# Performance work log

Measured on AMD Instinct MI355X. Metric: run time of the kernel, lower is better.

The kernel has to match this reference:

```python
import jax, jax.numpy as jnp
import numpy as np

B, S, D = 2, 2048, 2048
H, KV, HD = 32, 8, 64          # n_heads, n_kv_heads, head_dim
REP = H // KV                  # 4
THETA = 10000.0


def _rotate_half(u):
    h = u.shape[-1] // 2
    return jnp.concatenate([-u[..., h:], u[..., :h]], axis=-1)


def setup_inputs() -> dict:
    key = jax.random.key(0)
    ks = jax.random.split(key, 5)
    x = jax.random.normal(ks[0], (B, S, D), dtype=jnp.float32)
    Wq = jax.random.normal(ks[1], (D, H * HD), dtype=jnp.float32) * 0.02
    Wk = jax.random.normal(ks[2], (D, KV * HD), dtype=jnp.float32) * 0.02
    Wv = jax.random.normal(ks[3], (D, KV * HD), dtype=jnp.float32) * 0.02
    Wo = jax.random.normal(ks[4], (H * HD, D), dtype=jnp.float32) * 0.02
    return {"x": x, "Wq": Wq, "Wk": Wk, "Wv": Wv, "Wo": Wo}


def reference(x, Wq, Wk, Wv, Wo):
    b, s, d = x.shape
    # QKV projections (nn.Linear, no bias)
    q = (x @ Wq).reshape(b, s, H, HD).transpose(0, 2, 1, 3)   # [B,H,S,HD]
    k = (x @ Wk).reshape(b, s, KV, HD).transpose(0, 2, 1, 3)  # [B,KV,S,HD]
    v = (x @ Wv).reshape(b, s, KV, HD).transpose(0, 2, 1, 3)  # [B,KV,S,HD]

    # RoPE (position_offset = 0)
    inv_freq = 1.0 / (THETA ** (jnp.arange(0, HD, 2, dtype=jnp.float32) / HD))
    freqs = jnp.outer(jnp.arange(s, dtype=jnp.float32), inv_freq)  # [S,HD/2]
    emb = jnp.concatenate([freqs, freqs], axis=-1)                  # [S,HD]
    cos, sin = jnp.cos(emb), jnp.sin(emb)
    q = q * cos + _rotate_half(q) * sin
    k = k * cos + _rotate_half(k) * sin

    # Grouped attention: avoid materializing repeated KV tensors.
    qg = q.reshape(b, KV, REP, s, HD)                               # [B,KV,REP,S,HD]
    scale = 1.0 / np.sqrt(HD)
    scores = jnp.einsum('bgrqd,bgkd->bgrqk', qg, k) * scale         # [B,KV,REP,S,S]
    causal = jnp.tril(jnp.ones((s, s), dtype=bool))
    scores = jnp.where(causal, scores, jnp.finfo(jnp.float32).min)
    probs = jax.nn.softmax(scores.astype(jnp.float32), axis=-1).astype(q.dtype)
    out = jnp.einsum('bgrqk,bgkd->bgrqd', probs, v)                 # [B,KV,REP,S,HD]
    out = out.reshape(b, H, s, HD).transpose(0, 2, 1, 3).reshape(b, s, H * HD)
    return out @ Wo                                                  # [B,S,D]
```

## Files before the change

### kernel.cpp

```cpp
#include <hip/hip_runtime.h>
#include <math.h>

typedef __bf16 bf16_t;
typedef bf16_t bf16x8 __attribute__((ext_vector_type(8)));
typedef bf16_t bf16x4 __attribute__((ext_vector_type(4)));
typedef float floatx4 __attribute__((ext_vector_type(4)));
typedef short short4v __attribute__((ext_vector_type(4)));

#define MFMA16(a, b, c) __builtin_amdgcn_mfma_f32_16x16x32_bf16((a), (b), (c), 0, 0, 0)

#if __has_builtin(__builtin_amdgcn_exp2f)
#define PEXP(x) __builtin_amdgcn_exp2f(x)
#define SCORE_SCALE (0.125f * 1.4426950408889634f)
#else
#define PEXP(x) __expf(x)
#define SCORE_SCALE 0.125f
#endif

#if __has_builtin(__builtin_amdgcn_mfma_f32_16x16x16bf16_1k)
#define HAVE_MFMA_K16 1
__device__ __forceinline__ floatx4 mfma_k16(bf16x4 a, bf16x4 b, floatx4 c)
{
    union { bf16x4 v; short4v s; } ua, ub;
    ua.v = a; ub.v = b;
    return __builtin_amdgcn_mfma_f32_16x16x16bf16_1k(ua.s, ub.s, c, 0, 0, 0);
}
#endif

union PU { unsigned u[2]; bf16x4 v; };
union BU { unsigned u[4]; bf16x8 v; };

__device__ __forceinline__ void gld16(const void* g, void* lds)
{
    __builtin_amdgcn_global_load_lds(
        reinterpret_cast<const __attribute__((address_space(1))) void*>(
            reinterpret_cast<uintptr_t>(g)),
        reinterpret_cast<__attribute__((address_space(3))) void*>(
            (unsigned int)reinterpret_cast<uintptr_t>(lds)),
        16, 0, 0);
}

template <typename TC>
__device__ __forceinline__ void gemm_bt_body(
    const bf16_t* __restrict__ A, const bf16_t* __restrict__ Bt,
    TC* __restrict__ C, int row0, int col0, int N, int K,
    bf16_t* As, bf16_t* Bs)
{
    const int tid  = threadIdx.x;
    const int wave = tid >> 6, lane = tid & 63;
    const int quad = lane >> 4, l16 = lane & 15;
    const int wm = (wave >> 1) * 64, wn = (wave & 1) * 64;

    floatx4 acc[4][4] = {};

    for (int k0 = 0; k0 < K; k0 += 64) {
        __syncthreads();
        #pragma unroll
        for (int i = 0; i < 4; ++i) {
            int c = i * 256 + tid;
            int r = c >> 3, s = c & 7;
            int ks = k0 + ((s ^ (r & 7)) << 3);
            gld16(A  + (size_t)(row0 + r) * K + ks, &As[(i * 256 + wave * 64) * 8]);
            gld16(Bt + (size_t)(col0 + r) * K + ks, &Bs[(i * 256 + wave * 64) * 8]);
        }
        __syncthreads();
        #pragma unroll
        for (int kh = 0; kh < 2; ++kh) {
            bf16x8 af[4], bfr[4];
            #pragma unroll
            for (int t = 0; t < 4; ++t) {
                int ar = wm + t * 16 + l16;
                af[t]  = *(const bf16x8*)&As[ar * 64 + (((kh * 4 + quad) ^ (ar & 7)) << 3)];
                int br = wn + t * 16 + l16;
                bfr[t] = *(const bf16x8*)&Bs[br * 64 + (((kh * 4 + quad) ^ (br & 7)) << 3)];
            }
            #pragma unroll
            for (int mt = 0; mt < 4; ++mt)
                #pragma unroll
                for (int nt = 0; nt < 4; ++nt)
                    acc[mt][nt] = MFMA16(af[mt], bfr[nt], acc[mt][nt]);
        }
    }
    #pragma unroll
    for (int mt = 0; mt < 4; ++mt)
        #pragma unroll
        for (int nt = 0; nt < 4; ++nt)
            #pragma unroll
            for (int r = 0; r < 4; ++r)
                C[(size_t)(row0 + wm + mt * 16 + quad * 4 + r) * N
                  + col0 + wn + nt * 16 + l16] = (TC)acc[mt][nt][r];
}

template <typename TC>
__global__ __launch_bounds__(256) void gemm_bt(
    const bf16_t* __restrict__ A, const bf16_t* __restrict__ Bt,
    TC* __restrict__ C, int N, int K)
{
    __shared__ bf16_t As[128 * 64];
    __shared__ bf16_t Bs[128 * 64];
    gemm_bt_body<TC>(A, Bt, C, blockIdx.y * 128, blockIdx.x * 128, N, K, As, Bs);
}

__global__ __launch_bounds__(256) void gemm_qkv(
    const bf16_t* __restrict__ A, const bf16_t* __restrict__ BtQ,
    const bf16_t* __restrict__ BtK, const bf16_t* __restrict__ BtV,
    bf16_t* __restrict__ CQ, bf16_t* __restrict__ CK, bf16_t* __restrict__ CV)
{
    __shared__ bf16_t As[128 * 64];
    __shared__ bf16_t Bs[128 * 64];
    const int x = blockIdx.x;
    const bf16_t* Bt; bf16_t* C; int N, col0;
    if (x < 16)      { Bt = BtQ; C = CQ; N = 2048; col0 = x * 128; }
    else if (x < 20) { Bt = BtK; C = CK; N = 512;  col0 = (x - 16) * 128; }
    else             { Bt = BtV; C = CV; N = 512;  col0 = (x - 20) * 128; }
    gemm_bt_body<bf16_t>(A, Bt, C, blockIdx.y * 128, col0, N, 2048, As, Bs);
}

__device__ __forceinline__ void transpose_body(
    const float* __restrict__ W, bf16_t* __restrict__ Wt, int K, int N,
    int bx, int by, float (*t)[33], int tid)
{
    int tx = tid & 31, ty = tid >> 5;
    #pragma unroll
    for (int i = 0; i < 32; i += 8)
        t[ty + i][tx] = W[(size_t)(by + ty + i) * N + bx + tx];
    __syncthreads();
    #pragma unroll
    for (int i = 0; i < 32; i += 8)
        Wt[(size_t)(bx + ty + i) * K + by + tx] = (bf16_t)t[tx][ty + i];
}

__global__ __launch_bounds__(256) void prep_all(
    const float* __restrict__ x, const float* __restrict__ Wq,
    const float* __restrict__ Wk, const float* __restrict__ Wv,
    bf16_t* __restrict__ xb, bf16_t* __restrict__ WqT,
    bf16_t* __restrict__ WkT, bf16_t* __restrict__ WvT)
{
    __shared__ float t[32][33];
    const int blk = blockIdx.x, tid = threadIdx.x;
    if (blk < 8192) {
        int i = blk * 256 + tid;
        float4 f = ((const float4*)x)[i];
        bf16x4 v = {(bf16_t)f.x, (bf16_t)f.y, (bf16_t)f.z, (bf16_t)f.w};
        ((bf16x4*)xb)[i] = v;
    } else if (blk < 12288) {
        int r = blk - 8192;
        transpose_body(Wq, WqT, 2048, 2048, (r & 63) * 32, (r >> 6) * 32, t, tid);
    } else if (blk < 13312) {
        int r = blk - 12288;
        transpose_body(Wk, WkT, 2048, 512, (r & 15) * 32, (r >> 4) * 32, t, tid);
    } else {
        int r = blk - 13312;
        transpose_body(Wv, WvT, 2048, 512, (r & 15) * 32, (r >> 4) * 32, t, tid);
    }
}

__global__ __launch_bounds__(256) void mid_all(
    bf16_t* __restrict__ Kw, const bf16_t* __restrict__ Vw,
    bf16_t* __restrict__ VtG, const float* __restrict__ Wo,
    bf16_t* __restrict__ WoT)
{
    __shared__ float tf[32][33];
    __shared__ bf16_t tb[32][34];
    const int blk = blockIdx.x, tid = threadIdx.x;
    if (blk < 4096) {
        int idx = blk * 256 + tid;
        int i   = idx & 31;
        int h   = (idx >> 5) & 7;
        int row = idx >> 8;
        int pos = row & 2047;
        float invf = powf(10000.0f, -(float)i / 32.0f);
        float sv, cv;
        sincosf((float)pos * invf, &sv, &cv);
        size_t base = (size_t)row * 512 + (size_t)h * 64 + i;
        float a  = (float)Kw[base];
        float b2 = (float)Kw[base + 32];
        Kw[base]      = (bf16_t)(a * cv - b2 * sv);
        Kw[base + 32] = (bf16_t)(b2 * cv + a * sv);
    } else if (blk < 6144) {
        int r  = blk - 4096;
        int bz = r >> 10, r2 = r & 1023;
        int bx = (r2 & 15) * 32, by = (r2 >> 4) * 32;
        int tx = tid & 31, ty = tid >> 5;
        #pragma unroll
        for (int i = 0; i < 32; i += 8)
            tb[ty + i][tx] = Vw[((size_t)bz * 2048 + by + ty + i) * 512 + bx + tx];
        __syncthreads();
        #pragma unroll
        for (int i = 0; i < 32; i += 8)
            VtG[((size_t)bz * 512 + bx + ty + i) * 2048 + by + tx] = tb[tx][ty + i];
    } else {
        int r = blk - 6144;
        transpose_body(Wo, WoT, 2048, 2048, (r & 63) * 32, (r >> 6) * 32, tf, tid);
    }
}

__global__ __launch_bounds__(256) void gqa_attn(
    const bf16_t* __restrict__ Q, const bf16_t* __restrict__ Kc,
    const bf16_t* __restrict__ Vt, bf16_t* __restrict__ AO)
{
    __shared__ alignas(16) bf16_t Ks[2][64 * 64];
    __shared__ alignas(16) bf16_t Vs[2][64 * 64];

    const int x = blockIdx.x, h = blockIdx.y, b = blockIdx.z, g = h >> 2;
    const int tid  = threadIdx.x;
    const int wave = tid >> 6, lane = tid & 63;
    const int quad = lane >> 4, l16 = lane & 15;

    #pragma unroll 1
    for (int t = 0; t < 2; ++t) {
        const int qt = t ? x : (15 - x);
        const int q0 = qt * 128;
        int qb[2];
        qb[0] = q0 + wave * 16;
        qb[1] = qb[0] + 64;

        bf16x8 qf[2][2];
        #pragma unroll
        for (int mt = 0; mt < 2; ++mt) {
            int qrow = qb[mt] + l16;
            const bf16_t* qp = Q + (size_t)(b * 2048 + qrow) * 2048 + h * 64 + quad * 8;
            bf16x8 lo = *(const bf16x8*)qp;
            bf16x8 hi = *(const bf16x8*)(qp + 32);
            #pragma unroll
            for (int j = 0; j < 8; ++j) {
                int d = quad * 8 + j;
                float invf = powf(10000.0f, -(float)d / 32.0f);
                float sv, cv;
                sincosf((float)qrow * invf, &sv, &cv);
                float a = (float)lo[j], c2 = (float)hi[j];
                qf[mt][0][j] = (bf16_t)((a * cv - c2 * sv) * SCORE_SCALE);
                qf[mt][1][j] = (bf16_t)((c2 * cv + a * sv) * SCORE_SCALE);
            }
        }

        floatx4 o[2][4] = {};
        floatx4 ls4[2] = {};

        const int ktmax = 2 * qt + 1;

        __asm__ volatile("s_waitcnt lgkmcnt(0)" ::: "memory");
        __builtin_amdgcn_s_barrier();
        #pragma unroll
        for (int i = 0; i < 2; ++i) {
            int c = i * 256 + tid;
            int r = c >> 3, s = c & 7;
            int sw = (s ^ (r & 7)) << 3;
            gld16(Kc + (size_t)(b * 2048 + r) * 512 + g * 64 + sw,
                  &Ks[0][(i * 256 + wave * 64) * 8]);
            gld16(Vt + (size_t)(b * 512 + g * 64 + r) * 2048 + sw,
                  &Vs[0][(i * 256 + wave * 64) * 8]);
        }

        #pragma unroll 1
        for (int kt = 0; kt <= ktmax; ++kt) {
            const int cur = kt & 1;
            if (kt < ktmax) {
                const int kn = kt + 1;
                #pragma unroll
                for (int i = 0; i < 2; ++i) {
                    int c = i * 256 + tid;
                    int r = c >> 3, s = c & 7;
                    int sw = (s ^ (r & 7)) << 3;
                    gld16(Kc + (size_t)(b * 2048 + kn * 64 + r) * 512 + g * 64 + sw,
                          &Ks[cur ^ 1][(i * 256 + wave * 64) * 8]);
                    gld16(Vt + (size_t)(b * 512 + g * 64 + r) * 2048 + kn * 64 + sw,
                          &Vs[cur ^ 1][(i * 256 + wave * 64) * 8]);
                }
                __asm__ volatile("s_waitcnt vmcnt(4)" ::: "memory");
            } else {
                __asm__ volatile("s_waitcnt vmcnt(0)" ::: "memory");
            }
            __builtin_amdgcn_s_barrier();

            bool en[2];
            en[0] = (kt * 64) <= (qb[0] + 15);
            en[1] = (kt * 64) <= (qb[1] + 15);

            floatx4 st[2][4] = {};
            #pragma unroll
            for (int nt = 0; nt < 4; ++nt) {
                int kr = nt * 16 + l16;
                bf16x8 kf0 = *(const bf16x8*)&Ks[cur][kr * 64 + ((quad ^ (kr & 7)) << 3)];
                bf16x8 kf1 = *(const bf16x8*)&Ks[cur][kr * 64 + (((4 + quad) ^ (kr & 7)) << 3)];
                if (en[0]) {
                    st[0][nt] = MFMA16(kf0, qf[0][0], st[0][nt]);
                    st[0][nt] = MFMA16(kf1, qf[0][1], st[0][nt]);
                }
                if (en[1]) {
                    st[1][nt] = MFMA16(kf0, qf[1][0], st[1][nt]);
                    st[1][nt] = MFMA16(kf1, qf[1][1], st[1][nt]);
                }
            }

            PU pk[2][4];
            #pragma unroll
            for (int mt = 0; mt < 2; ++mt) {
                if (!en[mt]) continue;
                const bool diag = (kt * 64 + 63) > qb[mt];
                const int qa = qb[mt] + l16;
                #pragma unroll
                for (int nt = 0; nt < 4; ++nt) {
                    float pv[4];
                    #pragma unroll
                    for (int r = 0; r < 4; ++r) {
                        float e = PEXP(st[mt][nt][r]);
                        if (diag) {
                            int ka = kt * 64 + nt * 16 + quad * 4 + r;
                            if (ka > qa) e = 0.f;
                        }
                        ls4[mt][r] += e;
                        pv[r] = e;
                    }
                    pk[mt][nt].v = bf16x4{(bf16_t)pv[0], (bf16_t)pv[1],
                                          (bf16_t)pv[2], (bf16_t)pv[3]};
                }
            }

#ifdef HAVE_MFMA_K16
            #pragma unroll
            for (int nt = 0; nt < 4; ++nt)
                #pragma unroll
                for (int dt = 0; dt < 4; ++dt) {
                    int vr = dt * 16 + l16;
                    int slot = ((nt << 1) | (quad >> 1)) ^ (vr & 7);
                    bf16x4 va = *(const bf16x4*)&Vs[cur][vr * 64 + (slot << 3)
                                                         + ((quad & 1) << 2)];
                    if (en[0]) o[0][dt] = mfma_k16(va, pk[0][nt].v, o[0][dt]);
                    if (en[1]) o[1][dt] = mfma_k16(va, pk[1][nt].v, o[1][dt]);
                }
#else
            #pragma unroll
            for (int H = 0; H < 2; ++H) {
                BU bfv[2];
                #pragma unroll
                for (int mt = 0; mt < 2; ++mt) {
                    if (!en[mt]) continue;
                    #pragma unroll
                    for (int j = 0; j < 4; ++j) {
                        int srcl = (((quad & 1) << 1) + (j >> 1)) * 16 + l16;
                        unsigned a0 = (unsigned)__shfl((int)pk[mt][2 * H].u[j & 1], srcl, 64);
                        unsigned a1 = (unsigned)__shfl((int)pk[mt][2 * H + 1].u[j & 1], srcl, 64);
                        bfv[mt].u[j] = (quad >> 1) ? a1 : a0;
                    }
                }
                #pragma unroll
                for (int dt = 0; dt < 4; ++dt) {
                    int vr = dt * 16 + l16;
                    bf16x8 va = *(const bf16x8*)&Vs[cur][vr * 64
                                  + ((((H << 2) | quad) ^ (vr & 7)) << 3)];
                    if (en[0]) o[0][dt] = MFMA16(va, bfv[0].v, o[0][dt]);
                    if (en[1]) o[1][dt] = MFMA16(va, bfv[1].v, o[1][dt]);
                }
            }
#endif
            __asm__ volatile("s_waitcnt lgkmcnt(0)" ::: "memory");
            __builtin_amdgcn_s_barrier();
        }

        #pragma unroll
        for (int mt = 0; mt < 2; ++mt) {
            float l = ls4[mt][0] + ls4[mt][1] + ls4[mt][2] + ls4[mt][3];
            l += __shfl_xor(l, 16, 64);
            l += __shfl_xor(l, 32, 64);
            float rc = 1.0f / l;
            #pragma unroll
            for (int dt = 0; dt < 4; ++dt) {
                bf16x4 ov = {(bf16_t)(o[mt][dt][0] * rc), (bf16_t)(o[mt][dt][1] * rc),
                             (bf16_t)(o[mt][dt][2] * rc), (bf16_t)(o[mt][dt][3] * rc)};
                *(bf16x4*)&AO[(size_t)(b * 2048 + qb[mt] + l16) * 2048
                              + h * 64 + dt * 16 + quad * 4] = ov;
            }
        }
    }
}

extern "C" void kernel_launch(void* const* d_in, const int* in_sizes, int n_in,
                              void* d_out, int out_size, void* d_ws, size_t ws_size,
                              hipStream_t stream)
{
    const float* x  = (const float*)d_in[0];
    const float* Wq = (const float*)d_in[1];
    const float* Wk = (const float*)d_in[2];
    const float* Wv = (const float*)d_in[3];
    const float* Wo = (const float*)d_in[4];
    float* out = (float*)d_out;

    const size_t MB = 1024 * 1024;
    char* ws = (char*)d_ws;
    bf16_t* xb_AO = (bf16_t*)(ws);
    bf16_t* WqoT  = (bf16_t*)(ws + 16 * MB);
    bf16_t* WkT   = (bf16_t*)(ws + 24 * MB);
    bf16_t* WvT   = (bf16_t*)(ws + 26 * MB);
    bf16_t* Qw    = (bf16_t*)(ws + 28 * MB);
    bf16_t* Kw    = (bf16_t*)(ws + 44 * MB);
    bf16_t* Vw    = (bf16_t*)(ws + 48 * MB);
    bf16_t* VtG   = (bf16_t*)(ws + 52 * MB);

    prep_all<<<14336, 256, 0, stream>>>(x, Wq, Wk, Wv, xb_AO, WqoT, WkT, WvT);

    gemm_qkv<<<dim3(24, 32), 256, 0, stream>>>(xb_AO, WqoT, WkT, WvT, Qw, Kw, Vw);

    mid_all<<<10240, 256, 0, stream>>>(Kw, Vw, VtG, Wo, WqoT);

    gqa_attn<<<dim3(8, 32, 2), 256, 0, stream>>>(Qw, Kw, VtG, xb_AO);

    gemm_bt<float><<<dim3(16, 32), 256, 0, stream>>>(xb_AO, WqoT, out, 2048, 2048);
}
```

Before: 326.8 us.

## Use 256-row double-buffered GEMM tiles with async LDS prefetch for projections

Replaces the 128x128 single-buffered GEMM with a 512-thread, 256-row tile GEMM (256 or 128 columns) that double-buffers A/B tiles in dynamic LDS. The next k-slice is prefetched with global_load_lds while MFMAs run on the current one, using explicit vmcnt waits and raw barriers. MFMA issue priority is raised with setprio. The goal is to hide global load latency and raise reuse per LDS load. In exchange the kernel needs 128KB or 96KB of LDS, which limits occupancy, and launches fewer blocks (192 and 256), which may underfill the CUs.

```diff
diff --git a/kernel.cpp b/kernel.cpp
--- a/kernel.cpp
+++ b/kernel.cpp
@@ -40,80 +40,124 @@
         16, 0, 0);
 }
 
-template <typename TC>
-__device__ __forceinline__ void gemm_bt_body(
+template <int ROUNDS>
+__device__ __forceinline__ void stage512(
+    const bf16_t* __restrict__ g, int K, int row0, int k0,
+    bf16_t* lds, int tid, int wave)
+{
+    #pragma unroll
+    for (int i = 0; i < ROUNDS; ++i) {
+        int c = i * 512 + tid;
+        int r = c >> 3, s = c & 7;
+        gld16(g + (size_t)(row0 + r) * K + k0 + ((s ^ (r & 7)) << 3),
+              lds + (size_t)(i * 512 + wave * 64) * 8);
+    }
+}
+
+template <typename TC, int BN>
+__device__ __forceinline__ void gemm256_body(
     const bf16_t* __restrict__ A, const bf16_t* __restrict__ Bt,
-    TC* __restrict__ C, int row0, int col0, int N, int K,
-    bf16_t* As, bf16_t* Bs)
-{
+    TC* __restrict__ C, int row0, int col0, int N, int K, bf16_t* smem)
+{
+    constexpr int NT = BN / 64;
+    constexpr int RB = BN / 64;
+    constexpr int LPT = 4 + RB;
+
     const int tid  = threadIdx.x;
     const int wave = tid >> 6, lane = tid & 63;
     const int quad = lane >> 4, l16 = lane & 15;
-    const int wm = (wave >> 1) * 64, wn = (wave & 1) * 64;
-
-    floatx4 acc[4][4] = {};
-
-    for (int k0 = 0; k0 < K; k0 += 64) {
-        __syncthreads();
-        #pragma unroll
-        for (int i = 0; i < 4; ++i) {
-            int c = i * 256 + tid;
-            int r = c >> 3, s = c & 7;
-            int ks = k0 + ((s ^ (r & 7)) << 3);
-            gld16(A  + (size_t)(row0 + r) * K + ks, &As[(i * 256 + wave * 64) * 8]);
-            gld16(Bt + (size_t)(col0 + r) * K + ks, &Bs[(i * 256 + wave * 64) * 8]);
-        }
-        __syncthreads();
+    const int wm = (wave >> 2) * 128;
+    const int wn = (wave & 3) * (BN / 4);
+
+    bf16_t* As0 = smem;
+    bf16_t* As1 = smem + 256 * 64;
+    bf16_t* Bs0 = smem + 2 * 256 * 64;
+    bf16_t* Bs1 = Bs0 + BN * 64;
+
+    floatx4 acc[8][NT] = {};
+
+    const int ntile = K >> 6;
+
+    stage512<4>(A, K, row0, 0, As0, tid, wave);
+    stage512<RB>(Bt, K, col0, 0, Bs0, tid, wave);
+
+    #pragma unroll 1
+    for (int t = 0; t < ntile; ++t) {
+        const int cur = t & 1;
+        bf16_t* Asc = cur ? As1 : As0;
+        bf16_t* Bsc = cur ? Bs1 : Bs0;
+        bf16_t* Asn = cur ? As0 : As1;
+        bf16_t* Bsn = cur ? Bs0 : Bs1;
+
+        if (t + 1 < ntile) {
+            stage512<4>(A, K, row0, (t + 1) << 6, Asn, tid, wave);
+            stage512<RB>(Bt, K, col0, (t + 1) << 6, Bsn, tid, wave);
+            if constexpr (LPT == 8)
+                __asm__ volatile("s_waitcnt vmcnt(8)" ::: "memory");
+            else
+                __asm__ volatile("s_waitcnt vmcnt(6)" ::: "memory");
+        } else {
+            __asm__ volatile("s_waitcnt vmcnt(0)" ::: "memory");
+        }
+        __builtin_amdgcn_s_barrier();
+        __asm__ volatile("" ::: "memory");
+
         #pragma unroll
         for (int kh = 0; kh < 2; ++kh) {
-            bf16x8 af[4], bfr[4];
-            #pragma unroll
-            for (int t = 0; t < 4; ++t) {
-                int ar = wm + t * 16 + l16;
-                af[t]  = *(const bf16x8*)&As[ar * 64 + (((kh * 4 + quad) ^ (ar & 7)) << 3)];
-                int br = wn + t * 16 + l16;
-                bfr[t] = *(const bf16x8*)&Bs[br * 64 + (((kh * 4 + quad) ^ (br & 7)) << 3)];
-            }
-            #pragma unroll
-            for (int mt = 0; mt < 4; ++mt)
-                #pragma unroll
-                for (int nt = 0; nt < 4; ++nt)
+            bf16x8 af[8], bfr[NT];
+            #pragma unroll
+            for (int mt = 0; mt < 8; ++mt) {
+                int ar = wm + mt * 16 + l16;
+                af[mt] = *(const bf16x8*)&Asc[ar * 64 + (((kh * 4 + quad) ^ (ar & 7)) << 3)];
+            }
+            #pragma unroll
+            for (int nt = 0; nt < NT; ++nt) {
+                int br = wn + nt * 16 + l16;
+                bfr[nt] = *(const bf16x8*)&Bsc[br * 64 + (((kh * 4 + quad) ^ (br & 7)) << 3)];
+            }
+            __builtin_amdgcn_s_setprio(1);
+            #pragma unroll
+            for (int mt = 0; mt < 8; ++mt)
+                #pragma unroll
+                for (int nt = 0; nt < NT; ++nt)
                     acc[mt][nt] = MFMA16(af[mt], bfr[nt], acc[mt][nt]);
-        }
-    }
+            __builtin_amdgcn_s_setprio(0);
+        }
+        __asm__ volatile("s_waitcnt lgkmcnt(0)" ::: "memory");
+        __builtin_amdgcn_s_barrier();
+    }
+
     #pragma unroll
-    for (int mt = 0; mt < 4; ++mt)
-        #pragma unroll
-        for (int nt = 0; nt < 4; ++nt)
+    for (int mt = 0; mt < 8; ++mt)
+        #pragma unroll
+        for (int nt = 0; nt < NT; ++nt)
             #pragma unroll
             for (int r = 0; r < 4; ++r)
                 C[(size_t)(row0 + wm + mt * 16 + quad * 4 + r) * N
                   + col0 + wn + nt * 16 + l16] = (TC)acc[mt][nt][r];
 }
 
-template <typename TC>
-__global__ __launch_bounds__(256) void gemm_bt(
-    const bf16_t* __restrict__ A, const bf16_t* __restrict__ Bt,
-    TC* __restrict__ C, int N, int K)
-{
-    __shared__ bf16_t As[128 * 64];
-    __shared__ bf16_t Bs[128 * 64];
-    gemm_bt_body<TC>(A, Bt, C, blockIdx.y * 128, blockIdx.x * 128, N, K, As, Bs);
-}
-
-__global__ __launch_bounds__(256) void gemm_qkv(
+__global__ __launch_bounds__(512, 2) void gemm256_qkv(
     const bf16_t* __restrict__ A, const bf16_t* __restrict__ BtQ,
     const bf16_t* __restrict__ BtK, const bf16_t* __restrict__ BtV,
     bf16_t* __restrict__ CQ, bf16_t* __restrict__ CK, bf16_t* __restrict__ CV)
 {
-    __shared__ bf16_t As[128 * 64];
-    __shared__ bf16_t Bs[128 * 64];
+    extern __shared__ __align__(16) bf16_t smem[];
     const int x = blockIdx.x;
     const bf16_t* Bt; bf16_t* C; int N, col0;
-    if (x < 16)      { Bt = BtQ; C = CQ; N = 2048; col0 = x * 128; }
-    else if (x < 20) { Bt = BtK; C = CK; N = 512;  col0 = (x - 16) * 128; }
-    else             { Bt = BtV; C = CV; N = 512;  col0 = (x - 20) * 128; }
-    gemm_bt_body<bf16_t>(A, Bt, C, blockIdx.y * 128, col0, N, 2048, As, Bs);
+    if (x < 8)       { Bt = BtQ; C = CQ; N = 2048; col0 = x * 256; }
+    else if (x < 10) { Bt = BtK; C = CK; N = 512;  col0 = (x - 8) * 256; }
+    else             { Bt = BtV; C = CV; N = 512;  col0 = (x - 10) * 256; }
+    gemm256_body<bf16_t, 256>(A, Bt, C, blockIdx.y * 256, col0, N, 2048, smem);
+}
+
+__global__ __launch_bounds__(512, 2) void gemm256_out(
+    const bf16_t* __restrict__ A, const bf16_t* __restrict__ Bt,
+    float* __restrict__ C)
+{
+    extern __shared__ __align__(16) bf16_t smem[];
+    gemm256_body<float, 128>(A, Bt, C, blockIdx.y * 256, blockIdx.x * 128,
+                             2048, 2048, smem);
 }
 
 __device__ __forceinline__ void transpose_body(
@@ -397,13 +441,23 @@
     bf16_t* Vw    = (bf16_t*)(ws + 48 * MB);
     bf16_t* VtG   = (bf16_t*)(ws + 52 * MB);
 
+    static bool s_attr = false;
+    if (!s_attr) {
+        hipFuncSetAttribute(reinterpret_cast<const void*>(gemm256_qkv),
+                            hipFuncAttributeMaxDynamicSharedMemorySize, 131072);
+        hipFuncSetAttribute(reinterpret_cast<const void*>(gemm256_out),
+                            hipFuncAttributeMaxDynamicSharedMemorySize, 98304);
+        s_attr = true;
+    }
+
     prep_all<<<14336, 256, 0, stream>>>(x, Wq, Wk, Wv, xb_AO, WqoT, WkT, WvT);
 
-    gemm_qkv<<<dim3(24, 32), 256, 0, stream>>>(xb_AO, WqoT, WkT, WvT, Qw, Kw, Vw);
+    gemm256_qkv<<<dim3(12, 16), 512, 131072, stream>>>(
+        xb_AO, WqoT, WkT, WvT, Qw, Kw, Vw);
 
     mid_all<<<10240, 256, 0, stream>>>(Kw, Vw, VtG, Wo, WqoT);
 
     gqa_attn<<<dim3(8, 32, 2), 256, 0, stream>>>(Qw, Kw, VtG, xb_AO);
 
-    gemm_bt<float><<<dim3(16, 32), 256, 0, stream>>>(xb_AO, WqoT, out, 2048, 2048);
-}
+    gemm256_out<<<dim3(16, 16), 512, 98304, stream>>>(xb_AO, WqoT, out);
+}
```

Result: faster. 312.7 us (-4.3%).
